# Kernel tuning notes

Hardware: AMD Instinct MI355X
Metric: run time of the kernel (lower is better)

Reference implementation:

```python
import math
import jax, jax.numpy as jnp
import numpy as np

N = 50000       # num_nodes
D = 128         # input feature dim
OUT = 128       # output_dim
H = 8           # num_heads
F = OUT // H    # out_feats per head (= self_attn hidden_dim)
E_RAND = 800000 # random edges per graph (+ N self loops)
ALPHA = 0.8
BETA = 0.5


def _edges(key):
    k1, k2 = jax.random.split(key)
    src = jax.random.randint(k1, (E_RAND,), 0, N, dtype=jnp.int32)
    dst = jax.random.randint(k2, (E_RAND,), 0, N, dtype=jnp.int32)
    loop = jnp.arange(N, dtype=jnp.int32)  # dgl.add_self_loop
    return jnp.concatenate([src, loop]), jnp.concatenate([dst, loop])


def setup_inputs() -> dict:
    key = jax.random.key(0)
    ks = jax.random.split(key, 32)
    inp = {"x": jax.random.normal(ks[0], (N, D), jnp.float32)}
    inp["src_s"], inp["dst_s"] = _edges(ks[1])
    inp["src_t"], inp["dst_t"] = _edges(ks[2])
    inp["src_p"], inp["dst_p"] = _edges(ks[3])
    i = 4
    for v in ("s", "t", "p"):
        inp[f"W_{v}"] = jax.random.normal(ks[i], (OUT, D), jnp.float32) * 0.05; i += 1
        inp[f"al_{v}"] = jax.random.normal(ks[i], (H, F), jnp.float32) * 0.1; i += 1
        inp[f"ar_{v}"] = jax.random.normal(ks[i], (H, F), jnp.float32) * 0.1; i += 1
        inp[f"b_{v}"] = jnp.zeros((OUT,), jnp.float32)
    inp["Wq"] = jax.random.normal(ks[i], (F, OUT), jnp.float32) * 0.05; i += 1
    inp["bq"] = jnp.zeros((F,), jnp.float32)
    inp["Wk"] = jax.random.normal(ks[i], (F, OUT), jnp.float32) * 0.05; i += 1
    inp["bk"] = jnp.zeros((F,), jnp.float32)
    inp["Wm"] = jax.random.normal(ks[i], (1, N * OUT), jnp.float32) * 0.001; i += 1
    inp["bm"] = jnp.zeros((1,), jnp.float32)
    return inp


def _gat(x, src, dst, W, al, ar, b):
    # DGL GATConv (eval mode, negative_slope=0.2, activation=relu)
    feat = (x @ W.T).reshape(N, H, F)                      # [N,H,F]
    el = jnp.einsum('nhf,hf->nh', feat, al)                # [N,H]
    er = jnp.einsum('nhf,hf->nh', feat, ar)
    e = jax.nn.leaky_relu(el[src] + er[dst], 0.2)          # [E,H]
    m = jax.ops.segment_max(e, dst, num_segments=N)        # per-dst softmax
    ex = jnp.exp(e - m[dst])
    s = jax.ops.segment_sum(ex, dst, num_segments=N)
    attn = ex / s[dst]                                     # [E,H]
    out = jax.ops.segment_sum(feat[src] * attn[:, :, None], dst, num_segments=N)
    return jax.nn.relu(out + b.reshape(1, H, F)).reshape(N, OUT)


def reference(x, src_s, dst_s, src_t, dst_t, src_p, dst_p,
              W_s, al_s, ar_s, b_s, W_t, al_t, ar_t, b_t,
              W_p, al_p, ar_p, b_p, Wq, bq, Wk, bk, Wm, bm):
    s = _gat(x, src_s, dst_s, W_s, al_s, ar_s, b_s)
    t = _gat(x, src_t, dst_t, W_t, al_t, ar_t, b_t)
    p = _gat(x, src_p, dst_p, W_p, al_p, ar_p, b_p)
    views = jnp.stack([s, t, p])                           # [3,N,OUT]
    # self_attn: one scalar attention weight per view
    Q = jnp.einsum('vne,he->vnh', views, Wq) + bq          # [3,N,F]
    K = jnp.einsum('vne,he->vnh', views, Wk) + bk
    logits = jnp.sum(Q.reshape(3, -1) * K.reshape(3, -1), -1) / math.sqrt(F * N)
    w = jax.nn.softmax(logits)                             # [3]
    fused = w[:, None, None] * views
    views2 = ALPHA * fused + (1.0 - ALPHA) * views         # [3,N,OUT]
    # mv_attn: sigmoid-gated sum of views
    omega = jax.nn.sigmoid(views2.reshape(3, -1) @ Wm.T + bm)[:, 0]  # [3]
    mv = jnp.einsum('v,vne->ne', omega, views2)            # [N,OUT]
    result = BETA * views2 + (1.0 - BETA) * mv[None]       # [3,N,OUT]
    return mv, result
```

## Files before the change

kernel.cpp:

```cpp
#include <hip/hip_runtime.h>


#define N_NODES 50000
#define DIM 128
#define OUTD 128
#define NH 8
#define NF 16
#define NE 850000
#define NOFF 50001
#define NBUCK 49
#define BCAP 20480
#define BIN_EPT 8
#define BIN_EPB 2048

typedef float f32x4 __attribute__((ext_vector_type(4)));
typedef __bf16 bf16x8 __attribute__((ext_vector_type(8)));
typedef unsigned short u16x8 __attribute__((ext_vector_type(8)));

static __device__ __forceinline__ float bf2f_lo(unsigned int u) {
  return __uint_as_float(u << 16);
}
static __device__ __forceinline__ float bf2f_hi(unsigned int u) {
  return __uint_as_float(u & 0xffff0000u);
}
static __device__ __forceinline__ unsigned short f2bf(float f) {
  unsigned int u = __float_as_uint(f);
  unsigned int r = (u + 0x7fffu + ((u >> 16) & 1u)) >> 16;
  return (unsigned short)r;
}

__global__ __launch_bounds__(256) void gemm_feat_kernel(
    const float* __restrict__ x, const float* __restrict__ Ws,
    const float* __restrict__ Wt, const float* __restrict__ Wp,
    unsigned short* __restrict__ feat) {
  __shared__ unsigned short xa[128 * 128];
  __shared__ unsigned short wb[128 * 128];
  const int t = threadIdx.x;
  const int n0 = blockIdx.x * 128;

  for (int i = 0; i < 16; ++i) {
    int flat = (i * 256 + t) * 4;
    int r = flat >> 7, c = flat & 127;
    float4 val = make_float4(0.f, 0.f, 0.f, 0.f);
    if (n0 + r < N_NODES) val = *(const float4*)(x + (size_t)(n0 + r) * DIM + c);
    int byteoff = (r * 256 + c * 2) ^ ((r & 7) << 4);
    unsigned short* p = (unsigned short*)((char*)xa + byteoff);
    p[0] = f2bf(val.x); p[1] = f2bf(val.y); p[2] = f2bf(val.z); p[3] = f2bf(val.w);
  }

  const int wave = t >> 6, lane = t & 63;
  const int wr = wave >> 1, wc = wave & 1;
  const int lrow = lane & 15;
  const int kgrp = lane >> 4;

  for (int v = 0; v < 3; ++v) {
    const float* W = (v == 0) ? Ws : ((v == 1) ? Wt : Wp);
    __syncthreads();
    for (int i = 0; i < 16; ++i) {
      int flat = (i * 256 + t) * 4;
      int r = flat >> 7, c = flat & 127;
      float4 val = *(const float4*)(W + r * DIM + c);
      int byteoff = (r * 256 + c * 2) ^ ((r & 7) << 4);
      unsigned short* p = (unsigned short*)((char*)wb + byteoff);
      p[0] = f2bf(val.x); p[1] = f2bf(val.y); p[2] = f2bf(val.z); p[3] = f2bf(val.w);
    }
    __syncthreads();

    f32x4 acc[4][4];
    for (int m = 0; m < 4; ++m)
      for (int n = 0; n < 4; ++n) acc[m][n] = (f32x4)0.f;

    for (int ks = 0; ks < 4; ++ks) {
      bf16x8 af[4], bfr[4];
      int kb2 = (ks * 32 + kgrp * 8) * 2;
      for (int m = 0; m < 4; ++m) {
        int r = wr * 64 + m * 16 + lrow;
        af[m] = *(const bf16x8*)((const char*)xa + ((r * 256 + kb2) ^ ((r & 7) << 4)));
      }
      for (int n = 0; n < 4; ++n) {
        int r = wc * 64 + n * 16 + lrow;
        bfr[n] = *(const bf16x8*)((const char*)wb + ((r * 256 + kb2) ^ ((r & 7) << 4)));
      }
      for (int m = 0; m < 4; ++m)
        for (int n = 0; n < 4; ++n)
          acc[m][n] = __builtin_amdgcn_mfma_f32_16x16x32_bf16(af[m], bfr[n], acc[m][n], 0, 0, 0);
    }

    unsigned short* fv = feat + (size_t)v * N_NODES * OUTD;
    for (int m = 0; m < 4; ++m)
      for (int n = 0; n < 4; ++n) {
        int col = wc * 64 + n * 16 + lrow;
        for (int r4 = 0; r4 < 4; ++r4) {
          int row = n0 + wr * 64 + m * 16 + kgrp * 4 + r4;
          if (row < N_NODES) fv[(size_t)row * OUTD + col] = f2bf(acc[m][n][r4]);
        }
      }
  }
}

__global__ __launch_bounds__(256) void elr_kernel(
    const unsigned short* __restrict__ feat,
    const float* __restrict__ al_s, const float* __restrict__ ar_s,
    const float* __restrict__ al_t, const float* __restrict__ ar_t,
    const float* __restrict__ al_p, const float* __restrict__ ar_p,
    float* __restrict__ el, float* __restrict__ er) {
  int idx = blockIdx.x * 256 + threadIdx.x;
  if (idx >= 3 * N_NODES * NH) return;
  int v = idx / (N_NODES * NH);
  int rem = idx - v * (N_NODES * NH);
  int n = rem >> 3, h = rem & 7;
  const float* al = (v == 0) ? al_s : ((v == 1) ? al_t : al_p);
  const float* ar = (v == 0) ? ar_s : ((v == 1) ? ar_t : ar_p);
  const unsigned short* fr = feat + (size_t)v * N_NODES * OUTD + (size_t)n * OUTD + h * NF;
  uint4 a = *(const uint4*)(fr);
  uint4 b = *(const uint4*)(fr + 8);
  float fv[16];
  fv[0] = bf2f_lo(a.x); fv[1] = bf2f_hi(a.x); fv[2] = bf2f_lo(a.y); fv[3] = bf2f_hi(a.y);
  fv[4] = bf2f_lo(a.z); fv[5] = bf2f_hi(a.z); fv[6] = bf2f_lo(a.w); fv[7] = bf2f_hi(a.w);
  fv[8] = bf2f_lo(b.x); fv[9] = bf2f_hi(b.x); fv[10] = bf2f_lo(b.y); fv[11] = bf2f_hi(b.y);
  fv[12] = bf2f_lo(b.z); fv[13] = bf2f_hi(b.z); fv[14] = bf2f_lo(b.w); fv[15] = bf2f_hi(b.w);
  float accl = 0.f, accr = 0.f;
#pragma unroll
  for (int f = 0; f < NF; ++f) {
    accl += fv[f] * al[h * NF + f];
    accr += fv[f] * ar[h * NF + f];
  }
  el[idx] = accl;
  er[idx] = accr;
}

__global__ __launch_bounds__(256) void bin_kernel(
    const int* __restrict__ src_s, const int* __restrict__ dst_s,
    const int* __restrict__ src_t, const int* __restrict__ dst_t,
    const int* __restrict__ src_p, const int* __restrict__ dst_p,
    int* __restrict__ gtail, unsigned int* __restrict__ gbin) {
  const int v = blockIdx.y;
  const int* S = (v == 0) ? src_s : ((v == 1) ? src_t : src_p);
  const int* D = (v == 0) ? dst_s : ((v == 1) ? dst_t : dst_p);
  __shared__ int lhist[64], lbase[64];
  const int t = threadIdx.x;
  if (t < 64) lhist[t] = 0;
  __syncthreads();
  const int e0 = blockIdx.x * BIN_EPB + t * BIN_EPT;
  unsigned int pk[BIN_EPT];
  int bk[BIN_EPT], rk[BIN_EPT];
#pragma unroll
  for (int i = 0; i < BIN_EPT; ++i) {
    int e = e0 + i;
    if (e < NE) {
      unsigned int s = (unsigned int)S[e], d = (unsigned int)D[e];
      pk[i] = (s << 16) | d;
      bk[i] = (int)(d >> 10);
      rk[i] = atomicAdd(&lhist[bk[i]], 1);
    } else {
      bk[i] = -1;
    }
  }
  __syncthreads();
  if (t < 64) {
    int c = lhist[t];
    lbase[t] = (c > 0) ? atomicAdd(&gtail[v * 64 + t], c) : 0;
  }
  __syncthreads();
#pragma unroll
  for (int i = 0; i < BIN_EPT; ++i) {
    if (bk[i] >= 0) {
      int pos = lbase[bk[i]] + rk[i];
      if (pos < BCAP)
        gbin[((size_t)v * 64 + bk[i]) * BCAP + pos] = pk[i];
    }
  }
}

__global__ __launch_bounds__(256) void bucket_sort_kernel(
    const int* __restrict__ gtail, const unsigned int* __restrict__ gbin,
    int* __restrict__ offs, int* __restrict__ esrc) {
  __shared__ int lhist[1024];
  __shared__ int lcur[1024];
  __shared__ int wsum[4];
  __shared__ int sh_bbase;
  __shared__ unsigned int sorted[BCAP];
  const int v = blockIdx.y;
  const int b = blockIdx.x;
  const int t = threadIdx.x;
  const int wave = t >> 6, lane = t & 63;

  int cnt = gtail[v * 64 + b];
  if (cnt > BCAP) cnt = BCAP;
  const unsigned int* eb = gbin + ((size_t)v * 64 + b) * BCAP;

  if (t < 64) {
    int valb = (t < b) ? gtail[v * 64 + t] : 0;
#pragma unroll
    for (int m = 1; m < 64; m <<= 1) valb += __shfl_xor(valb, m, 64);
    if (t == 0) sh_bbase = valb;
  }
  lhist[t] = 0; lhist[t + 256] = 0; lhist[t + 512] = 0; lhist[t + 768] = 0;
  __syncthreads();

  for (int e = t; e < cnt; e += 256)
    atomicAdd(&lhist[eb[e] & 1023u], 1);
  __syncthreads();

  const int i0 = t * 4;
  int c0 = lhist[i0], c1 = lhist[i0 + 1], c2 = lhist[i0 + 2], c3 = lhist[i0 + 3];
  int s = c0 + c1 + c2 + c3;
  int incl = s;
#pragma unroll
  for (int st = 1; st < 64; st <<= 1) {
    int o = __shfl_up(incl, st, 64);
    if (lane >= st) incl += o;
  }
  if (lane == 63) wsum[wave] = incl;
  __syncthreads();
  if (t == 0) {
    int a = 0;
#pragma unroll
    for (int i = 0; i < 4; ++i) { int tmp = wsum[i]; wsum[i] = a; a += tmp; }
  }
  __syncthreads();
  const int base0 = wsum[wave] + (incl - s);
  lhist[i0] = base0;
  lhist[i0 + 1] = base0 + c0;
  lhist[i0 + 2] = base0 + c0 + c1;
  lhist[i0 + 3] = base0 + c0 + c1 + c2;
  lcur[i0] = base0;
  lcur[i0 + 1] = base0 + c0;
  lcur[i0 + 2] = base0 + c0 + c1;
  lcur[i0 + 3] = base0 + c0 + c1 + c2;

  const int bbase = sh_bbase;
  if (b == 0 && t == 0) offs[v * NOFF] = 0;
  {
    int n = b * 1024 + i0;
    int in0 = base0 + c0, in1 = in0 + c1, in2 = in1 + c2, in3 = in2 + c3;
    if (n + 0 < N_NODES) offs[v * NOFF + n + 1] = bbase + in0;
    if (n + 1 < N_NODES) offs[v * NOFF + n + 2] = bbase + in1;
    if (n + 2 < N_NODES) offs[v * NOFF + n + 3] = bbase + in2;
    if (n + 3 < N_NODES) offs[v * NOFF + n + 4] = bbase + in3;
  }
  __syncthreads();

  for (int e = t; e < cnt; e += 256) {
    unsigned int pk = eb[e];
    int pos = atomicAdd(&lcur[pk & 1023u], 1);
    sorted[pos] = pk >> 16;
  }
  __syncthreads();

  int* ev = esrc + (size_t)v * NE + bbase;
  for (int e = t; e < cnt; e += 256) ev[e] = (int)sorted[e];
}

__global__ __launch_bounds__(256) void gat_kernel(
    const int* __restrict__ offs, const int* __restrict__ esrc,
    const float* __restrict__ el, const float* __restrict__ er,
    const unsigned short* __restrict__ feat,
    const float* __restrict__ b_s, const float* __restrict__ b_t,
    const float* __restrict__ b_p, float* __restrict__ views) {
  const int v = blockIdx.y;
  const int n = blockIdx.x * 4 + (threadIdx.x >> 6);
  const int lane = threadIdx.x & 63;
  const int g = lane >> 4;
  const int q = lane & 15;
  const int h = q >> 1;
  const int* off_v = offs + v * NOFF;
  const int off0 = off_v[n];
  const int deg = off_v[n + 1] - off0;
  const int* es = esrc + (size_t)v * NE + off0;
  const float* el_v = el + (size_t)v * N_NODES * NH;
  const float er_h = er[((size_t)v * N_NODES + n) * NH + h];
  const unsigned short* featv = feat + (size_t)v * N_NODES * OUTD;

  float acc[8];
#pragma unroll
  for (int j = 0; j < 8; ++j) acc[j] = 0.f;
  float sm = 0.f;

  for (int base = 0; base < deg; base += 8) {
    int e0 = base + g, e1 = base + 4 + g;
    bool v0 = e0 < deg, v1 = e1 < deg;
    int s0 = es[v0 ? e0 : 0];
    int s1 = es[v1 ? e1 : 0];
    float val0 = el_v[s0 * NH + h] + er_h;
    float val1 = el_v[s1 * NH + h] + er_h;
    uint4 pk0 = *(const uint4*)(featv + s0 * OUTD + q * 8);
    uint4 pk1 = *(const uint4*)(featv + s1 * OUTD + q * 8);
    val0 = (val0 > 0.f) ? val0 : 0.2f * val0;
    val1 = (val1 > 0.f) ? val1 : 0.2f * val1;
    float aw0 = v0 ? __expf(val0) : 0.f;
    float aw1 = v1 ? __expf(val1) : 0.f;
    sm += aw0 + aw1;
    acc[0] += aw0 * bf2f_lo(pk0.x) + aw1 * bf2f_lo(pk1.x);
    acc[1] += aw0 * bf2f_hi(pk0.x) + aw1 * bf2f_hi(pk1.x);
    acc[2] += aw0 * bf2f_lo(pk0.y) + aw1 * bf2f_lo(pk1.y);
    acc[3] += aw0 * bf2f_hi(pk0.y) + aw1 * bf2f_hi(pk1.y);
    acc[4] += aw0 * bf2f_lo(pk0.z) + aw1 * bf2f_lo(pk1.z);
    acc[5] += aw0 * bf2f_hi(pk0.z) + aw1 * bf2f_hi(pk1.z);
    acc[6] += aw0 * bf2f_lo(pk0.w) + aw1 * bf2f_lo(pk1.w);
    acc[7] += aw0 * bf2f_hi(pk0.w) + aw1 * bf2f_hi(pk1.w);
  }

#pragma unroll
  for (int m = 16; m < 64; m <<= 1) {
    sm += __shfl_xor(sm, m, 64);
#pragma unroll
    for (int j = 0; j < 8; ++j) acc[j] += __shfl_xor(acc[j], m, 64);
  }

  if (g == 0) {
    const float inv = 1.0f / sm;
    const float* bv = (v == 0) ? b_s : ((v == 1) ? b_t : b_p);
    float r[8];
#pragma unroll
    for (int j = 0; j < 8; ++j) {
      float x = acc[j] * inv + bv[q * 8 + j];
      r[j] = (x > 0.f) ? x : 0.f;
    }
    float* dst = views + (size_t)v * N_NODES * OUTD + (size_t)n * OUTD + q * 8;
    *(float4*)(dst) = make_float4(r[0], r[1], r[2], r[3]);
    *(float4*)(dst + 4) = make_float4(r[4], r[5], r[6], r[7]);
  }
}

__global__ __launch_bounds__(256) void viewred_kernel(
    const float* __restrict__ views, const float* __restrict__ Wq,
    const float* __restrict__ bq, const float* __restrict__ Wk,
    const float* __restrict__ bk, const float* __restrict__ Wm,
    float* __restrict__ logits, float* __restrict__ dsum) {
  __shared__ unsigned short vt[128 * 128];
  __shared__ unsigned short wq[16 * 128];
  __shared__ unsigned short wk[16 * 128];
  __shared__ float redq[4], redd[4];
  const int v = blockIdx.y;
  const int n0 = blockIdx.x * 128;
  const int t = threadIdx.x;
  const float* Vv = views + (size_t)v * N_NODES * OUTD;

  {
    int flat = t * 8;
    int r = flat >> 7, c = flat & 127;
    int byteoff = (r * 256 + c * 2) ^ ((r & 7) << 4);
    float4 qa = *(const float4*)(Wq + flat);
    float4 qb = *(const float4*)(Wq + flat + 4);
    u16x8 oq;
    oq[0] = f2bf(qa.x); oq[1] = f2bf(qa.y); oq[2] = f2bf(qa.z); oq[3] = f2bf(qa.w);
    oq[4] = f2bf(qb.x); oq[5] = f2bf(qb.y); oq[6] = f2bf(qb.z); oq[7] = f2bf(qb.w);
    *(u16x8*)((char*)wq + byteoff) = oq;
    float4 ka = *(const float4*)(Wk + flat);
    float4 kb = *(const float4*)(Wk + flat + 4);
    u16x8 ok;
    ok[0] = f2bf(ka.x); ok[1] = f2bf(ka.y); ok[2] = f2bf(ka.z); ok[3] = f2bf(ka.w);
    ok[4] = f2bf(kb.x); ok[5] = f2bf(kb.y); ok[6] = f2bf(kb.z); ok[7] = f2bf(kb.w);
    *(u16x8*)((char*)wk + byteoff) = ok;
  }

  float dp = 0.f;
  for (int i = 0; i < 8; ++i) {
    int flat = (i * 256 + t) * 8;
    int r = flat >> 7, c = flat & 127;
    int row = n0 + r;
    u16x8 o = (u16x8)0;
    if (row < N_NODES) {
      size_t goff = (size_t)row * OUTD + c;
      float4 a = *(const float4*)(Vv + goff);
      float4 b = *(const float4*)(Vv + goff + 4);
      float4 wa = *(const float4*)(Wm + goff);
      float4 wb2 = *(const float4*)(Wm + goff + 4);
      dp += a.x * wa.x + a.y * wa.y + a.z * wa.z + a.w * wa.w;
      dp += b.x * wb2.x + b.y * wb2.y + b.z * wb2.z + b.w * wb2.w;
      o[0] = f2bf(a.x); o[1] = f2bf(a.y); o[2] = f2bf(a.z); o[3] = f2bf(a.w);
      o[4] = f2bf(b.x); o[5] = f2bf(b.y); o[6] = f2bf(b.z); o[7] = f2bf(b.w);
    }
    int byteoff = (r * 256 + c * 2) ^ ((r & 7) << 4);
    *(u16x8*)((char*)vt + byteoff) = o;
  }
  __syncthreads();

  const int wave = t >> 6, lane = t & 63;
  const int lrow = lane & 15;
  const int kgrp = lane >> 4;
  const float bqv = bq[lrow];
  const float bkv = bk[lrow];
  float qk = 0.f;

  f32x4 accQ[2], accK[2];
  accQ[0] = (f32x4)0.f; accQ[1] = (f32x4)0.f;
  accK[0] = (f32x4)0.f; accK[1] = (f32x4)0.f;
  for (int ks = 0; ks < 4; ++ks) {
    int kb2 = (ks * 32 + kgrp * 8) * 2;
    int rb = lrow;
    bf16x8 bqf = *(const bf16x8*)((const char*)wq + ((rb * 256 + kb2) ^ ((rb & 7) << 4)));
    bf16x8 bkf = *(const bf16x8*)((const char*)wk + ((rb * 256 + kb2) ^ ((rb & 7) << 4)));
#pragma unroll
    for (int m = 0; m < 2; ++m) {
      int r = (wave * 2 + m) * 16 + lrow;
      bf16x8 af = *(const bf16x8*)((const char*)vt + ((r * 256 + kb2) ^ ((r & 7) << 4)));
      accQ[m] = __builtin_amdgcn_mfma_f32_16x16x32_bf16(af, bqf, accQ[m], 0, 0, 0);
      accK[m] = __builtin_amdgcn_mfma_f32_16x16x32_bf16(af, bkf, accK[m], 0, 0, 0);
    }
  }
#pragma unroll
  for (int m = 0; m < 2; ++m) {
#pragma unroll
    for (int j = 0; j < 4; ++j) {
      int row = n0 + (wave * 2 + m) * 16 + kgrp * 4 + j;
      if (row < N_NODES) qk += (accQ[m][j] + bqv) * (accK[m][j] + bkv);
    }
  }

#pragma unroll
  for (int m = 1; m < 64; m <<= 1) {
    qk += __shfl_xor(qk, m, 64);
    dp += __shfl_xor(dp, m, 64);
  }
  if (lane == 0) { redq[wave] = qk; redd[wave] = dp; }
  __syncthreads();
  if (t == 0) {
    atomicAdd(&logits[v], redq[0] + redq[1] + redq[2] + redq[3]);
    atomicAdd(&dsum[v], redd[0] + redd[1] + redd[2] + redd[3]);
  }
}

__global__ void scalar_kernel(const float* __restrict__ logits,
                              const float* __restrict__ dsum,
                              const float* __restrict__ bm, float* __restrict__ gc) {
  if (threadIdx.x == 0 && blockIdx.x == 0) {
    const float scale = 1.0f / sqrtf((float)(NF * N_NODES));
    float l0 = logits[0] * scale, l1 = logits[1] * scale, l2 = logits[2] * scale;
    float mx = fmaxf(l0, fmaxf(l1, l2));
    float e0 = __expf(l0 - mx), e1 = __expf(l1 - mx), e2 = __expf(l2 - mx);
    float inv = 1.0f / (e0 + e1 + e2);
    float g0 = 0.8f * e0 * inv + 0.2f;
    float g1 = 0.8f * e1 * inv + 0.2f;
    float g2 = 0.8f * e2 * inv + 0.2f;
    float bmv = bm[0];
    float o0 = 1.0f / (1.0f + __expf(-(g0 * dsum[0] + bmv)));
    float o1 = 1.0f / (1.0f + __expf(-(g1 * dsum[1] + bmv)));
    float o2 = 1.0f / (1.0f + __expf(-(g2 * dsum[2] + bmv)));
    gc[0] = g0; gc[1] = g1; gc[2] = g2;
    gc[3] = o0 * g0; gc[4] = o1 * g1; gc[5] = o2 * g2;
  }
}

__global__ __launch_bounds__(256) void final_kernel(
    const float* __restrict__ views, const float* __restrict__ gc,
    float* __restrict__ out) {
  const size_t NT = (size_t)N_NODES * OUTD;
  size_t base = ((size_t)blockIdx.x * 256 + threadIdx.x) * 4;
  if (base >= NT) return;
  float g0 = gc[0], g1 = gc[1], g2 = gc[2], c0 = gc[3], c1 = gc[4], c2 = gc[5];
  float4 a0 = *(const float4*)(views + base);
  float4 a1 = *(const float4*)(views + NT + base);
  float4 a2 = *(const float4*)(views + 2 * NT + base);
  float4 mv;
  mv.x = c0 * a0.x + c1 * a1.x + c2 * a2.x;
  mv.y = c0 * a0.y + c1 * a1.y + c2 * a2.y;
  mv.z = c0 * a0.z + c1 * a1.z + c2 * a2.z;
  mv.w = c0 * a0.w + c1 * a1.w + c2 * a2.w;
  *(float4*)(out + base) = mv;
  float4 r;
  r.x = 0.5f * (g0 * a0.x) + 0.5f * mv.x;
  r.y = 0.5f * (g0 * a0.y) + 0.5f * mv.y;
  r.z = 0.5f * (g0 * a0.z) + 0.5f * mv.z;
  r.w = 0.5f * (g0 * a0.w) + 0.5f * mv.w;
  *(float4*)(out + NT + base) = r;
  r.x = 0.5f * (g1 * a1.x) + 0.5f * mv.x;
  r.y = 0.5f * (g1 * a1.y) + 0.5f * mv.y;
  r.z = 0.5f * (g1 * a1.z) + 0.5f * mv.z;
  r.w = 0.5f * (g1 * a1.w) + 0.5f * mv.w;
  *(float4*)(out + 2 * NT + base) = r;
  r.x = 0.5f * (g2 * a2.x) + 0.5f * mv.x;
  r.y = 0.5f * (g2 * a2.y) + 0.5f * mv.y;
  r.z = 0.5f * (g2 * a2.z) + 0.5f * mv.z;
  r.w = 0.5f * (g2 * a2.w) + 0.5f * mv.w;
  *(float4*)(out + 3 * NT + base) = r;
}

extern "C" void kernel_launch(void* const* d_in, const int* in_sizes, int n_in,
                              void* d_out, int out_size, void* d_ws, size_t ws_size,
                              hipStream_t stream) {
  const float* x = (const float*)d_in[0];
  const int* src_s = (const int*)d_in[1];
  const int* dst_s = (const int*)d_in[2];
  const int* src_t = (const int*)d_in[3];
  const int* dst_t = (const int*)d_in[4];
  const int* src_p = (const int*)d_in[5];
  const int* dst_p = (const int*)d_in[6];
  const float* W_s = (const float*)d_in[7];
  const float* al_s = (const float*)d_in[8];
  const float* ar_s = (const float*)d_in[9];
  const float* b_s = (const float*)d_in[10];
  const float* W_t = (const float*)d_in[11];
  const float* al_t = (const float*)d_in[12];
  const float* ar_t = (const float*)d_in[13];
  const float* b_t = (const float*)d_in[14];
  const float* W_p = (const float*)d_in[15];
  const float* al_p = (const float*)d_in[16];
  const float* ar_p = (const float*)d_in[17];
  const float* b_p = (const float*)d_in[18];
  const float* Wq = (const float*)d_in[19];
  const float* bq = (const float*)d_in[20];
  const float* Wk = (const float*)d_in[21];
  const float* bk = (const float*)d_in[22];
  const float* Wm = (const float*)d_in[23];
  const float* bm = (const float*)d_in[24];
  float* out = (float*)d_out;

  char* ws = (char*)d_ws;
  unsigned short* feat = (unsigned short*)ws;
  float* el = (float*)(ws + 38400000);
  float* er = (float*)(ws + 43200000);
  float* views = (float*)(ws + 48000000);
  int* offs = (int*)(ws + 124800000);
  int* esrc = (int*)(ws + 126000016);
  int* gtail = (int*)(ws + 136800016);
  float* scal = (float*)(ws + 136800784);

  unsigned int* gbin = (unsigned int*)(ws + 49000000);

  hipMemsetAsync(gtail, 0, 768 + 48, stream);

  gemm_feat_kernel<<<dim3(391), dim3(256), 0, stream>>>(x, W_s, W_t, W_p, feat);
  elr_kernel<<<dim3((3 * N_NODES * NH + 255) / 256), dim3(256), 0, stream>>>(
      feat, al_s, ar_s, al_t, ar_t, al_p, ar_p, el, er);
  bin_kernel<<<dim3((NE + BIN_EPB - 1) / BIN_EPB, 3), dim3(256), 0, stream>>>(
      src_s, dst_s, src_t, dst_t, src_p, dst_p, gtail, gbin);
  bucket_sort_kernel<<<dim3(NBUCK, 3), dim3(256), 0, stream>>>(
      gtail, gbin, offs, esrc);
  gat_kernel<<<dim3(12500, 3), dim3(256), 0, stream>>>(
      offs, esrc, el, er, feat, b_s, b_t, b_p, views);
  viewred_kernel<<<dim3(391, 3), dim3(256), 0, stream>>>(
      views, Wq, bq, Wk, bk, Wm, scal, scal + 3);
  scalar_kernel<<<dim3(1), dim3(64), 0, stream>>>(scal, scal + 3, bm, scal + 6);
  final_kernel<<<dim3(6250), dim3(256), 0, stream>>>(views, scal + 6, out);
}
```

Before: 445.9 us.

## Prefetch gat edges, per-wave bin histograms, 1024-thread bucket sort, fused view loop

The GAT aggregation loop now software-prefetches the next batch of edge sources, el values and bf16 features before computing the current batch, and uses packed float2 accumulators. bin_kernel keeps per-wave local histograms so fewer lanes contend on the same LDS atomics. bucket_sort runs with 1024 threads per block using a one-bin-per-thread scan. viewred processes all three views in a single block loop, loading the Wq/Wk tiles once per block instead of once per view. Together these aim to hide gather latency and cut LDS contention, at the cost of more registers and fewer, longer viewred blocks.

Measured after the change: 418.9 us. -6.1%, faster.

```diff
diff --git a/kernel.cpp b/kernel.cpp
--- a/kernel.cpp
+++ b/kernel.cpp
@@ -14,6 +14,7 @@
 #define BIN_EPB 2048
 
 typedef float f32x4 __attribute__((ext_vector_type(4)));
+typedef float f32x2 __attribute__((ext_vector_type(2)));
 typedef __bf16 bf16x8 __attribute__((ext_vector_type(8)));
 typedef unsigned short u16x8 __attribute__((ext_vector_type(8)));
 
@@ -22,6 +23,12 @@
 }
 static __device__ __forceinline__ float bf2f_hi(unsigned int u) {
   return __uint_as_float(u & 0xffff0000u);
+}
+static __device__ __forceinline__ f32x2 up2(unsigned int u) {
+  f32x2 r;
+  r.x = __uint_as_float(u << 16);
+  r.y = __uint_as_float(u & 0xffff0000u);
+  return r;
 }
 static __device__ __forceinline__ unsigned short f2bf(float f) {
   unsigned int u = __float_as_uint(f);
@@ -137,9 +144,10 @@
   const int v = blockIdx.y;
   const int* S = (v == 0) ? src_s : ((v == 1) ? src_t : src_p);
   const int* D = (v == 0) ? dst_s : ((v == 1) ? dst_t : dst_p);
-  __shared__ int lhist[64], lbase[64];
+  __shared__ int lhist[4][64], lbase[4][64];
   const int t = threadIdx.x;
-  if (t < 64) lhist[t] = 0;
+  const int wave = t >> 6;
+  ((int*)lhist)[t] = 0;
   __syncthreads();
   const int e0 = blockIdx.x * BIN_EPB + t * BIN_EPT;
   unsigned int pk[BIN_EPT];
@@ -151,35 +159,40 @@
       unsigned int s = (unsigned int)S[e], d = (unsigned int)D[e];
       pk[i] = (s << 16) | d;
       bk[i] = (int)(d >> 10);
-      rk[i] = atomicAdd(&lhist[bk[i]], 1);
+      rk[i] = atomicAdd(&lhist[wave][bk[i]], 1);
     } else {
       bk[i] = -1;
     }
   }
   __syncthreads();
   if (t < 64) {
-    int c = lhist[t];
-    lbase[t] = (c > 0) ? atomicAdd(&gtail[v * 64 + t], c) : 0;
+    int c0 = lhist[0][t], c1 = lhist[1][t], c2 = lhist[2][t], c3 = lhist[3][t];
+    int tot = c0 + c1 + c2 + c3;
+    int gb = (tot > 0) ? atomicAdd(&gtail[v * 64 + t], tot) : 0;
+    lbase[0][t] = gb;
+    lbase[1][t] = gb + c0;
+    lbase[2][t] = gb + c0 + c1;
+    lbase[3][t] = gb + c0 + c1 + c2;
   }
   __syncthreads();
 #pragma unroll
   for (int i = 0; i < BIN_EPT; ++i) {
     if (bk[i] >= 0) {
-      int pos = lbase[bk[i]] + rk[i];
+      int pos = lbase[wave][bk[i]] + rk[i];
       if (pos < BCAP)
         gbin[((size_t)v * 64 + bk[i]) * BCAP + pos] = pk[i];
     }
   }
 }
 
-__global__ __launch_bounds__(256) void bucket_sort_kernel(
+__global__ __launch_bounds__(1024) void bucket_sort_kernel(
     const int* __restrict__ gtail, const unsigned int* __restrict__ gbin,
     int* __restrict__ offs, int* __restrict__ esrc) {
-  __shared__ int lhist[1024];
   __shared__ int lcur[1024];
-  __shared__ int wsum[4];
+  __shared__ int wsum[16];
   __shared__ int sh_bbase;
   __shared__ unsigned int sorted[BCAP];
+  __shared__ int lhist[1024];
   const int v = blockIdx.y;
   const int b = blockIdx.x;
   const int t = threadIdx.x;
@@ -195,17 +208,15 @@
     for (int m = 1; m < 64; m <<= 1) valb += __shfl_xor(valb, m, 64);
     if (t == 0) sh_bbase = valb;
   }
-  lhist[t] = 0; lhist[t + 256] = 0; lhist[t + 512] = 0; lhist[t + 768] = 0;
-  __syncthreads();
-
-  for (int e = t; e < cnt; e += 256)
+  lhist[t] = 0;
+  __syncthreads();
+
+  for (int e = t; e < cnt; e += 1024)
     atomicAdd(&lhist[eb[e] & 1023u], 1);
   __syncthreads();
 
-  const int i0 = t * 4;
-  int c0 = lhist[i0], c1 = lhist[i0 + 1], c2 = lhist[i0 + 2], c3 = lhist[i0 + 3];
-  int s = c0 + c1 + c2 + c3;
-  int incl = s;
+  int val = lhist[t];
+  int incl = val;
 #pragma unroll
   for (int st = 1; st < 64; st <<= 1) {
     int o = __shfl_up(incl, st, 64);
@@ -213,35 +224,29 @@
   }
   if (lane == 63) wsum[wave] = incl;
   __syncthreads();
-  if (t == 0) {
-    int a = 0;
-#pragma unroll
-    for (int i = 0; i < 4; ++i) { int tmp = wsum[i]; wsum[i] = a; a += tmp; }
-  }
-  __syncthreads();
-  const int base0 = wsum[wave] + (incl - s);
-  lhist[i0] = base0;
-  lhist[i0 + 1] = base0 + c0;
-  lhist[i0 + 2] = base0 + c0 + c1;
-  lhist[i0 + 3] = base0 + c0 + c1 + c2;
-  lcur[i0] = base0;
-  lcur[i0 + 1] = base0 + c0;
-  lcur[i0 + 2] = base0 + c0 + c1;
-  lcur[i0 + 3] = base0 + c0 + c1 + c2;
+  if (t < 64) {
+    int wv = (lane < 16) ? wsum[lane] : 0;
+    int winc = wv;
+#pragma unroll
+    for (int st = 1; st < 16; st <<= 1) {
+      int o = __shfl_up(winc, st, 64);
+      if (lane >= st) winc += o;
+    }
+    if (lane < 16) wsum[lane] = winc - wv;
+  }
+  __syncthreads();
+  const int base = wsum[wave] + incl - val;
+  lcur[t] = base;
 
   const int bbase = sh_bbase;
   if (b == 0 && t == 0) offs[v * NOFF] = 0;
   {
-    int n = b * 1024 + i0;
-    int in0 = base0 + c0, in1 = in0 + c1, in2 = in1 + c2, in3 = in2 + c3;
-    if (n + 0 < N_NODES) offs[v * NOFF + n + 1] = bbase + in0;
-    if (n + 1 < N_NODES) offs[v * NOFF + n + 2] = bbase + in1;
-    if (n + 2 < N_NODES) offs[v * NOFF + n + 3] = bbase + in2;
-    if (n + 3 < N_NODES) offs[v * NOFF + n + 4] = bbase + in3;
-  }
-  __syncthreads();
-
-  for (int e = t; e < cnt; e += 256) {
+    int n = b * 1024 + t;
+    if (n < N_NODES) offs[v * NOFF + n + 1] = bbase + base + val;
+  }
+  __syncthreads();
+
+  for (int e = t; e < cnt; e += 1024) {
     unsigned int pk = eb[e];
     int pos = atomicAdd(&lcur[pk & 1023u], 1);
     sorted[pos] = pk >> 16;
@@ -249,7 +254,7 @@
   __syncthreads();
 
   int* ev = esrc + (size_t)v * NE + bbase;
-  for (int e = t; e < cnt; e += 256) ev[e] = (int)sorted[e];
+  for (int e = t; e < cnt; e += 1024) ev[e] = (int)sorted[e];
 }
 
 __global__ __launch_bounds__(256) void gat_kernel(
@@ -272,40 +277,56 @@
   const float er_h = er[((size_t)v * N_NODES + n) * NH + h];
   const unsigned short* featv = feat + (size_t)v * N_NODES * OUTD;
 
-  float acc[8];
-#pragma unroll
-  for (int j = 0; j < 8; ++j) acc[j] = 0.f;
+  f32x2 acc2[4];
+#pragma unroll
+  for (int j = 0; j < 4; ++j) acc2[j] = (f32x2)0.f;
   float sm = 0.f;
 
+  int e0 = g, e1 = 4 + g;
+  bool v0 = e0 < deg, v1 = e1 < deg;
+  int s0 = es[v0 ? e0 : 0];
+  int s1 = es[v1 ? e1 : 0];
+  float l0 = el_v[s0 * NH + h];
+  float l1 = el_v[s1 * NH + h];
+  uint4 pk0 = *(const uint4*)(featv + (size_t)s0 * OUTD + q * 8);
+  uint4 pk1 = *(const uint4*)(featv + (size_t)s1 * OUTD + q * 8);
+
   for (int base = 0; base < deg; base += 8) {
-    int e0 = base + g, e1 = base + 4 + g;
-    bool v0 = e0 < deg, v1 = e1 < deg;
-    int s0 = es[v0 ? e0 : 0];
-    int s1 = es[v1 ? e1 : 0];
-    float val0 = el_v[s0 * NH + h] + er_h;
-    float val1 = el_v[s1 * NH + h] + er_h;
-    uint4 pk0 = *(const uint4*)(featv + s0 * OUTD + q * 8);
-    uint4 pk1 = *(const uint4*)(featv + s1 * OUTD + q * 8);
-    val0 = (val0 > 0.f) ? val0 : 0.2f * val0;
-    val1 = (val1 > 0.f) ? val1 : 0.2f * val1;
-    float aw0 = v0 ? __expf(val0) : 0.f;
-    float aw1 = v1 ? __expf(val1) : 0.f;
+    bool cv0 = v0, cv1 = v1;
+    float cl0 = l0, cl1 = l1;
+    uint4 cp0 = pk0, cp1 = pk1;
+    int nb = base + 8;
+    if (nb < deg) {
+      e0 = nb + g; e1 = nb + 4 + g;
+      v0 = e0 < deg; v1 = e1 < deg;
+      s0 = es[v0 ? e0 : 0];
+      s1 = es[v1 ? e1 : 0];
+      l0 = el_v[s0 * NH + h];
+      l1 = el_v[s1 * NH + h];
+      pk0 = *(const uint4*)(featv + (size_t)s0 * OUTD + q * 8);
+      pk1 = *(const uint4*)(featv + (size_t)s1 * OUTD + q * 8);
+    }
+    float val0 = cl0 + er_h;
+    float val1 = cl1 + er_h;
+    val0 = fmaxf(val0, 0.2f * val0);
+    val1 = fmaxf(val1, 0.2f * val1);
+    float aw0 = cv0 ? __expf(val0) : 0.f;
+    float aw1 = cv1 ? __expf(val1) : 0.f;
     sm += aw0 + aw1;
-    acc[0] += aw0 * bf2f_lo(pk0.x) + aw1 * bf2f_lo(pk1.x);
-    acc[1] += aw0 * bf2f_hi(pk0.x) + aw1 * bf2f_hi(pk1.x);
-    acc[2] += aw0 * bf2f_lo(pk0.y) + aw1 * bf2f_lo(pk1.y);
-    acc[3] += aw0 * bf2f_hi(pk0.y) + aw1 * bf2f_hi(pk1.y);
-    acc[4] += aw0 * bf2f_lo(pk0.z) + aw1 * bf2f_lo(pk1.z);
-    acc[5] += aw0 * bf2f_hi(pk0.z) + aw1 * bf2f_hi(pk1.z);
-    acc[6] += aw0 * bf2f_lo(pk0.w) + aw1 * bf2f_lo(pk1.w);
-    acc[7] += aw0 * bf2f_hi(pk0.w) + aw1 * bf2f_hi(pk1.w);
+    acc2[0] += aw0 * up2(cp0.x) + aw1 * up2(cp1.x);
+    acc2[1] += aw0 * up2(cp0.y) + aw1 * up2(cp1.y);
+    acc2[2] += aw0 * up2(cp0.z) + aw1 * up2(cp1.z);
+    acc2[3] += aw0 * up2(cp0.w) + aw1 * up2(cp1.w);
   }
 
 #pragma unroll
   for (int m = 16; m < 64; m <<= 1) {
     sm += __shfl_xor(sm, m, 64);
 #pragma unroll
-    for (int j = 0; j < 8; ++j) acc[j] += __shfl_xor(acc[j], m, 64);
+    for (int j = 0; j < 4; ++j) {
+      acc2[j].x += __shfl_xor(acc2[j].x, m, 64);
+      acc2[j].y += __shfl_xor(acc2[j].y, m, 64);
+    }
   }
 
   if (g == 0) {
@@ -313,9 +334,11 @@
     const float* bv = (v == 0) ? b_s : ((v == 1) ? b_t : b_p);
     float r[8];
 #pragma unroll
-    for (int j = 0; j < 8; ++j) {
-      float x = acc[j] * inv + bv[q * 8 + j];
-      r[j] = (x > 0.f) ? x : 0.f;
+    for (int j = 0; j < 4; ++j) {
+      float x0 = acc2[j].x * inv + bv[q * 8 + 2 * j];
+      float x1 = acc2[j].y * inv + bv[q * 8 + 2 * j + 1];
+      r[2 * j] = (x0 > 0.f) ? x0 : 0.f;
+      r[2 * j + 1] = (x1 > 0.f) ? x1 : 0.f;
     }
     float* dst = views + (size_t)v * N_NODES * OUTD + (size_t)n * OUTD + q * 8;
     *(float4*)(dst) = make_float4(r[0], r[1], r[2], r[3]);
@@ -332,10 +355,11 @@
   __shared__ unsigned short wq[16 * 128];
   __shared__ unsigned short wk[16 * 128];
   __shared__ float redq[4], redd[4];
-  const int v = blockIdx.y;
   const int n0 = blockIdx.x * 128;
   const int t = threadIdx.x;
-  const float* Vv = views + (size_t)v * N_NODES * OUTD;
+  const int wave = t >> 6, lane = t & 63;
+  const int lrow = lane & 15;
+  const int kgrp = lane >> 4;
 
   {
     int flat = t * 8;
@@ -355,70 +379,71 @@
     *(u16x8*)((char*)wk + byteoff) = ok;
   }
 
-  float dp = 0.f;
-  for (int i = 0; i < 8; ++i) {
-    int flat = (i * 256 + t) * 8;
-    int r = flat >> 7, c = flat & 127;
-    int row = n0 + r;
-    u16x8 o = (u16x8)0;
-    if (row < N_NODES) {
-      size_t goff = (size_t)row * OUTD + c;
-      float4 a = *(const float4*)(Vv + goff);
-      float4 b = *(const float4*)(Vv + goff + 4);
-      float4 wa = *(const float4*)(Wm + goff);
-      float4 wb2 = *(const float4*)(Wm + goff + 4);
-      dp += a.x * wa.x + a.y * wa.y + a.z * wa.z + a.w * wa.w;
-      dp += b.x * wb2.x + b.y * wb2.y + b.z * wb2.z + b.w * wb2.w;
-      o[0] = f2bf(a.x); o[1] = f2bf(a.y); o[2] = f2bf(a.z); o[3] = f2bf(a.w);
-      o[4] = f2bf(b.x); o[5] = f2bf(b.y); o[6] = f2bf(b.z); o[7] = f2bf(b.w);
-    }
-    int byteoff = (r * 256 + c * 2) ^ ((r & 7) << 4);
-    *(u16x8*)((char*)vt + byteoff) = o;
-  }
-  __syncthreads();
-
-  const int wave = t >> 6, lane = t & 63;
-  const int lrow = lane & 15;
-  const int kgrp = lane >> 4;
   const float bqv = bq[lrow];
   const float bkv = bk[lrow];
-  float qk = 0.f;
-
-  f32x4 accQ[2], accK[2];
-  accQ[0] = (f32x4)0.f; accQ[1] = (f32x4)0.f;
-  accK[0] = (f32x4)0.f; accK[1] = (f32x4)0.f;
-  for (int ks = 0; ks < 4; ++ks) {
-    int kb2 = (ks * 32 + kgrp * 8) * 2;
-    int rb = lrow;
-    bf16x8 bqf = *(const bf16x8*)((const char*)wq + ((rb * 256 + kb2) ^ ((rb & 7) << 4)));
-    bf16x8 bkf = *(const bf16x8*)((const char*)wk + ((rb * 256 + kb2) ^ ((rb & 7) << 4)));
+
+  for (int v = 0; v < 3; ++v) {
+    const float* Vv = views + (size_t)v * N_NODES * OUTD;
+    float dp = 0.f;
+    for (int i = 0; i < 8; ++i) {
+      int flat = (i * 256 + t) * 8;
+      int r = flat >> 7, c = flat & 127;
+      int row = n0 + r;
+      u16x8 o = (u16x8)0;
+      if (row < N_NODES) {
+        size_t goff = (size_t)row * OUTD + c;
+        float4 a = *(const float4*)(Vv + goff);
+        float4 b = *(const float4*)(Vv + goff + 4);
+        float4 wa = *(const float4*)(Wm + goff);
+        float4 wb2 = *(const float4*)(Wm + goff + 4);
+        dp += a.x * wa.x + a.y * wa.y + a.z * wa.z + a.w * wa.w;
+        dp += b.x * wb2.x + b.y * wb2.y + b.z * wb2.z + b.w * wb2.w;
+        o[0] = f2bf(a.x); o[1] = f2bf(a.y); o[2] = f2bf(a.z); o[3] = f2bf(a.w);
+        o[4] = f2bf(b.x); o[5] = f2bf(b.y); o[6] = f2bf(b.z); o[7] = f2bf(b.w);
+      }
+      int byteoff = (r * 256 + c * 2) ^ ((r & 7) << 4);
+      *(u16x8*)((char*)vt + byteoff) = o;
+    }
+    __syncthreads();
+
+    float qk = 0.f;
+    f32x4 accQ[2], accK[2];
+    accQ[0] = (f32x4)0.f; accQ[1] = (f32x4)0.f;
+    accK[0] = (f32x4)0.f; accK[1] = (f32x4)0.f;
+    for (int ks = 0; ks < 4; ++ks) {
+      int kb2 = (ks * 32 + kgrp * 8) * 2;
+      int rb = lrow;
+      bf16x8 bqf = *(const bf16x8*)((const char*)wq + ((rb * 256 + kb2) ^ ((rb & 7) << 4)));
+      bf16x8 bkf = *(const bf16x8*)((const char*)wk + ((rb * 256 + kb2) ^ ((rb & 7) << 4)));
+#pragma unroll
+      for (int m = 0; m < 2; ++m) {
+        int r = (wave * 2 + m) * 16 + lrow;
+        bf16x8 af = *(const bf16x8*)((const char*)vt + ((r * 256 + kb2) ^ ((r & 7) << 4)));
+        accQ[m] = __builtin_amdgcn_mfma_f32_16x16x32_bf16(af, bqf, accQ[m], 0, 0, 0);
+        accK[m] = __builtin_amdgcn_mfma_f32_16x16x32_bf16(af, bkf, accK[m], 0, 0, 0);
+      }
+    }
 #pragma unroll
     for (int m = 0; m < 2; ++m) {
-      int r = (wave * 2 + m) * 16 + lrow;
-      bf16x8 af = *(const bf16x8*)((const char*)vt + ((r * 256 + kb2) ^ ((r & 7) << 4)));
-      accQ[m] = __builtin_amdgcn_mfma_f32_16x16x32_bf16(af, bqf, accQ[m], 0, 0, 0);
-      accK[m] = __builtin_amdgcn_mfma_f32_16x16x32_bf16(af, bkf, accK[m], 0, 0, 0);
-    }
-  }
-#pragma unroll
-  for (int m = 0; m < 2; ++m) {
-#pragma unroll
-    for (int j = 0; j < 4; ++j) {
-      int row = n0 + (wave * 2 + m) * 16 + kgrp * 4 + j;
-      if (row < N_NODES) qk += (accQ[m][j] + bqv) * (accK[m][j] + bkv);
-    }
-  }
-
-#pragma unroll
-  for (int m = 1; m < 64; m <<= 1) {
-    qk += __shfl_xor(qk, m, 64);
-    dp += __shfl_xor(dp, m, 64);
-  }
-  if (lane == 0) { redq[wave] = qk; redd[wave] = dp; }
-  __syncthreads();
-  if (t == 0) {
-    atomicAdd(&logits[v], redq[0] + redq[1] + redq[2] + redq[3]);
-    atomicAdd(&dsum[v], redd[0] + redd[1] + redd[2] + redd[3]);
+#pragma unroll
+      for (int j = 0; j < 4; ++j) {
+        int row = n0 + (wave * 2 + m) * 16 + kgrp * 4 + j;
+        if (row < N_NODES) qk += (accQ[m][j] + bqv) * (accK[m][j] + bkv);
+      }
+    }
+
+#pragma unroll
+    for (int m = 1; m < 64; m <<= 1) {
+      qk += __shfl_xor(qk, m, 64);
+      dp += __shfl_xor(dp, m, 64);
+    }
+    if (lane == 0) { redq[wave] = qk; redd[wave] = dp; }
+    __syncthreads();
+    if (t == 0) {
+      atomicAdd(&logits[v], redq[0] + redq[1] + redq[2] + redq[3]);
+      atomicAdd(&dsum[v], redd[0] + redd[1] + redd[2] + redd[3]);
+    }
+    __syncthreads();
   }
 }
 
@@ -526,11 +551,11 @@
       feat, al_s, ar_s, al_t, ar_t, al_p, ar_p, el, er);
   bin_kernel<<<dim3((NE + BIN_EPB - 1) / BIN_EPB, 3), dim3(256), 0, stream>>>(
       src_s, dst_s, src_t, dst_t, src_p, dst_p, gtail, gbin);
-  bucket_sort_kernel<<<dim3(NBUCK, 3), dim3(256), 0, stream>>>(
+  bucket_sort_kernel<<<dim3(NBUCK, 3), dim3(1024), 0, stream>>>(
       gtail, gbin, offs, esrc);
   gat_kernel<<<dim3(12500, 3), dim3(256), 0, stream>>>(
       offs, esrc, el, er, feat, b_s, b_t, b_p, views);
-  viewred_kernel<<<dim3(391, 3), dim3(256), 0, stream>>>(
+  viewred_kernel<<<dim3(391), dim3(256), 0, stream>>>(
       views, Wq, bq, Wk, bk, Wm, scal, scal + 3);
   scalar_kernel<<<dim3(1), dim3(64), 0, stream>>>(scal, scal + 3, bm, scal + 6);
   final_kernel<<<dim3(6250), dim3(256), 0, stream>>>(views, scal + 6, out);
```
